# Kernel tuning notes

Hardware: AMD Instinct MI355X
Metric: run time of the kernel (lower is better)

Reference implementation:

```python
import jax, jax.numpy as jnp
import numpy as np

N_ATOM_TYPES = 100
N_BOND_TYPES = 10
N_NODES = 10000
N_EDGES = 320000
N_CAND = 100000
HID = 256
N_MP = 3


def setup_inputs() -> dict:
    key = jax.random.key(0)
    ks = jax.random.split(key, 16)
    d = HID
    inp = {
        "atom_types": jax.random.randint(ks[0], (N_NODES,), 0, N_ATOM_TYPES),
        "bond_types": jax.random.randint(ks[1], (N_EDGES,), 0, N_BOND_TYPES),
        "edge_index": jax.random.randint(ks[2], (2, N_EDGES), 0, N_NODES),
        "candidates": jax.random.randint(ks[3], (N_CAND, 2), 0, N_NODES),
        # parameters (weights stored as [in, out]; bias [out])
        "atom_embed": jax.random.normal(ks[4], (N_ATOM_TYPES, d)) * 0.02,
        "atom_W": jax.random.normal(ks[5], (d, d)) / np.sqrt(d),
        "atom_b": jnp.zeros((d,)),
        "bond_embed": jax.random.normal(ks[6], (N_BOND_TYPES, d)) * 0.02,
        "bond_W": jax.random.normal(ks[7], (d, d)) / np.sqrt(d),
        "bond_b": jnp.zeros((d,)),
        "conv_W": jax.random.normal(ks[8], (N_MP, d, d)) / np.sqrt(d),
        "conv_b": jnp.zeros((N_MP, d)),
        "s_W1": jax.random.normal(ks[9], (2 * d, d)) / np.sqrt(2 * d),
        "s_b1": jnp.zeros((d,)),
        "s_W2": jax.random.normal(ks[10], (d, 1)) / np.sqrt(d),
        "s_b2": jnp.zeros((1,)),
    }
    return inp


def _wln_forward(atom_types, bond_types, edge_index, candidates,
                 atom_embed, atom_W, atom_b, bond_embed, bond_W, bond_b,
                 conv_W, conv_b, s_W1, s_b1, s_W2, s_b2):
    # encoders
    h = atom_embed[atom_types] @ atom_W + atom_b            # [N, d]
    e = bond_embed[bond_types] @ bond_W + bond_b            # [E, d] (unused downstream, as in the original forward)
    del e

    src, dst = edge_index[0], edge_index[1]
    n = h.shape[0]
    ones = jnp.ones((src.shape[0],), dtype=h.dtype)
    deg_out = jax.ops.segment_sum(ones, src, num_segments=n)
    deg_in = jax.ops.segment_sum(ones, dst, num_segments=n)
    norm_src = jnp.where(deg_out > 0, deg_out ** -0.5, 0.0)[:, None]  # [N,1]
    norm_dst = jnp.where(deg_in > 0, deg_in ** -0.5, 0.0)[:, None]

    # message passing: DGL GraphConv norm='both' + ReLU
    for i in range(conv_W.shape[0]):
        m = (h * norm_src)[src]                             # [E, d]
        agg = jax.ops.segment_sum(m, dst, num_segments=n)   # [N, d]
        h = jax.nn.relu((agg * norm_dst) @ conv_W[i] + conv_b[i])

    # batched candidate scorer: gather + concat + 2-layer MLP
    u, v = candidates[:, 0], candidates[:, 1]
    pair = jnp.concatenate([h[u], h[v]], axis=-1)           # [C, 2d]
    hid = jax.nn.relu(pair @ s_W1 + s_b1)                   # [C, d]
    scores = hid @ s_W2 + s_b2                              # [C, 1]
    return scores.squeeze(-1)                               # [C]


def reference(atom_types, bond_types, edge_index, candidates,
              atom_embed, atom_W, atom_b, bond_embed, bond_W, bond_b,
              conv_W, conv_b, s_W1, s_b1, s_W2, s_b2):
    return _wln_forward(atom_types, bond_types, edge_index, candidates,
                        atom_embed, atom_W, atom_b, bond_embed, bond_W, bond_b,
                        conv_W, conv_b, s_W1, s_b1, s_W2, s_b2)
```

## Files before the change

kernel.cpp:

```cpp
#include <hip/hip_runtime.h>

#define N_NODES 10000
#define N_EDGES 320000
#define N_CAND  100000
#define HID     256
#define N_MP    3
#define N_ATYPE 100

static __device__ __forceinline__ float relu_f(float x) { return x > 0.f ? x : 0.f; }

static __device__ __forceinline__ void gemm_core(
    const float* __restrict__ A, const float* __restrict__ B,
    const float* __restrict__ bias, const float* __restrict__ scale,
    float* __restrict__ C, int M, int mb, int nb,
    int kbase, int klen, int doRelu)
{
    __shared__ float As[32][64];
    __shared__ float Bs[32][64];

    int tid = threadIdx.x;
    int tx = tid & 15;
    int ty = tid >> 4;

    float acc[4][4] = {};

    for (int k0 = kbase; k0 < kbase + klen; k0 += 32) {
        #pragma unroll
        for (int p = 0; p < 2; ++p) {
            int flat = p * 256 + tid;
            int row  = flat >> 3;
            int kc   = flat & 7;
            float4 av = make_float4(0.f, 0.f, 0.f, 0.f);
            if (mb + row < M)
                av = *(const float4*)(A + (size_t)(mb + row) * 256 + k0 + kc * 4);
            int sc = row ^ (kc << 2);
            As[kc * 4 + 0][sc] = av.x;
            As[kc * 4 + 1][sc] = av.y;
            As[kc * 4 + 2][sc] = av.z;
            As[kc * 4 + 3][sc] = av.w;
        }
        #pragma unroll
        for (int p = 0; p < 2; ++p) {
            int flat = p * 256 + tid;
            int row  = flat >> 4;
            int c    = flat & 15;
            *(float4*)(&Bs[row][c * 4]) =
                *(const float4*)(B + (size_t)(k0 + row) * 256 + nb + c * 4);
        }
        __syncthreads();

        #pragma unroll 16
        for (int k = 0; k < 32; ++k) {
            float4 a4 = *(const float4*)(&As[k][(ty * 4) ^ ((k >> 2) << 2)]);
            float4 b4 = *(const float4*)(&Bs[k][tx * 4]);
            float a[4] = {a4.x, a4.y, a4.z, a4.w};
            float b[4] = {b4.x, b4.y, b4.z, b4.w};
            #pragma unroll
            for (int i = 0; i < 4; ++i)
                #pragma unroll
                for (int j = 0; j < 4; ++j)
                    acc[i][j] = fmaf(a[i], b[j], acc[i][j]);
        }
        __syncthreads();
    }

    float bvv[4] = {0.f, 0.f, 0.f, 0.f};
    if (bias) {
        float4 bv = *(const float4*)(bias + nb + tx * 4);
        bvv[0] = bv.x; bvv[1] = bv.y; bvv[2] = bv.z; bvv[3] = bv.w;
    }
    #pragma unroll
    for (int i = 0; i < 4; ++i) {
        int row = mb + ty * 4 + i;
        if (row >= M) continue;
        float sc = scale ? scale[row] : 1.0f;
        float r[4];
        #pragma unroll
        for (int j = 0; j < 4; ++j) {
            r[j] = acc[i][j] + bvv[j];
            if (doRelu) r[j] = relu_f(r[j]);
            r[j] *= sc;
        }
        *(float4*)(C + (size_t)row * 256 + nb + tx * 4) =
            make_float4(r[0], r[1], r[2], r[3]);
    }
}

__global__ __launch_bounds__(256) void k_gemm(
    const float* __restrict__ A, const float* __restrict__ B,
    const float* __restrict__ bias, float* __restrict__ C,
    int M, int doRelu)
{
    gemm_core(A, B, bias, nullptr, C, M, blockIdx.x * 64, blockIdx.y * 64,
              0, 256, doRelu);
}

__global__ __launch_bounds__(256) void k_gemm_conv(
    const float* __restrict__ A, const float* __restrict__ B,
    float* __restrict__ C0, float* __restrict__ C1, int M)
{
    int bid = blockIdx.x;
    int l = bid & 7;
    int r = bid >> 3;
    int ks = r & 1;
    int y  = (r >> 1) & 3;
    int g  = r >> 3;
    int x  = g * 8 + l;
    if (x * 64 >= M) return;
    float* C = ks ? C1 : C0;
    gemm_core(A, B, nullptr, nullptr, C, M, x * 64, y * 64, ks * 128, 128, 0);
}

__global__ __launch_bounds__(256) void k_combine(
    float* __restrict__ C0, const float* __restrict__ C1,
    const float* __restrict__ bias, const float* __restrict__ scale)
{
    int i = blockIdx.x * 256 + threadIdx.x;
    if (i >= N_NODES * 64) return;
    int row  = i >> 6;
    int col4 = i & 63;
    float4 a = ((const float4*)C0)[i];
    float4 b = ((const float4*)C1)[i];
    float4 bv = ((const float4*)bias)[col4];
    float sc = scale ? scale[row] : 1.0f;
    float4 r;
    r.x = relu_f(a.x + b.x + bv.x) * sc;
    r.y = relu_f(a.y + b.y + bv.y) * sc;
    r.z = relu_f(a.z + b.z + bv.z) * sc;
    r.w = relu_f(a.w + b.w + bv.w) * sc;
    ((float4*)C0)[i] = r;
}

__global__ __launch_bounds__(256) void k_gemm_pq(
    const float* __restrict__ A, const float* __restrict__ W1,
    float* __restrict__ P, float* __restrict__ Q, int M)
{
    int bid = blockIdx.x;
    int l = bid & 7;
    int r = bid >> 3;
    int y = r & 7;
    int g = r >> 3;
    int x = g * 8 + l;
    if (x * 64 >= M) return;
    int half = y >> 2;
    const float* B = W1 + (size_t)half * 256 * 256;
    float* C = half ? Q : P;
    gemm_core(A, B, nullptr, nullptr, C, M, x * 64, (y & 3) * 64, 0, 256, 0);
}

__global__ void k_hist(const int* __restrict__ ei,
                       int* __restrict__ dout, int* __restrict__ din)
{
    int e = blockIdx.x * blockDim.x + threadIdx.x;
    if (e >= N_EDGES) return;
    atomicAdd(&dout[ei[e]], 1);
    atomicAdd(&din[ei[N_EDGES + e]], 1);
}

__global__ void k_norm(const int* __restrict__ dout, const int* __restrict__ din,
                       float* __restrict__ ns, float* __restrict__ nd)
{
    int i = blockIdx.x * blockDim.x + threadIdx.x;
    if (i >= N_NODES) return;
    int o = dout[i], in = din[i];
    ns[i] = (o  > 0) ? (1.0f / sqrtf((float)o))  : 0.f;
    nd[i] = (in > 0) ? (1.0f / sqrtf((float)in)) : 0.f;
}

__global__ __launch_bounds__(256) void k_h0(const int* __restrict__ types,
                                            const float* __restrict__ E0,
                                            const float* __restrict__ ns,
                                            float* __restrict__ h)
{
    int node = blockIdx.x * 4 + (threadIdx.x >> 6);
    int lane = threadIdx.x & 63;
    if (node >= N_NODES) return;
    int t = types[node];
    float s = ns[node];
    float4 v = ((const float4*)E0)[t * 64 + lane];
    v.x *= s; v.y *= s; v.z *= s; v.w *= s;
    ((float4*)h)[node * 64 + lane] = v;
}

__global__ __launch_bounds__(1024) void k_scan(const int* __restrict__ deg,
                                               int* __restrict__ off, int n)
{
    __shared__ int part[1024];
    int t = threadIdx.x;
    int chunk = (n + 1023) / 1024;
    int base = t * chunk;
    int s = 0;
    for (int i = 0; i < chunk; ++i) {
        int idx = base + i;
        if (idx < n) s += deg[idx];
    }
    part[t] = s;
    __syncthreads();
    for (int d = 1; d < 1024; d <<= 1) {
        int v = (t >= d) ? part[t - d] : 0;
        __syncthreads();
        part[t] += v;
        __syncthreads();
    }
    int run = (t == 0) ? 0 : part[t - 1];
    if (t == 0) off[0] = 0;
    for (int i = 0; i < chunk; ++i) {
        int idx = base + i;
        if (idx < n) { run += deg[idx]; off[idx + 1] = run; }
    }
}

__global__ void k_fill(const int* __restrict__ ei, const int* __restrict__ off,
                       int* __restrict__ cur, int* __restrict__ csr)
{
    int e = blockIdx.x * blockDim.x + threadIdx.x;
    if (e >= N_EDGES) return;
    int d = ei[N_EDGES + e];
    int p = off[d] + atomicAdd(&cur[d], 1);
    csr[p] = ei[e];
}

__global__ __launch_bounds__(256) void k_agg(
    const float* __restrict__ h, const float* __restrict__ nd,
    const int* __restrict__ off, const int* __restrict__ csr,
    float* __restrict__ out)
{
    int bid  = blockIdx.x;
    int slot = bid & 7;
    int c    = slot >> 1;
    int p    = ((bid >> 3) << 1) | (slot & 1);
    int wave = threadIdx.x >> 6;
    int lane = threadIdx.x & 63;
    int wi   = p * 4 + wave;
    int col  = c * 64 + lane;

    for (int node = wi; node < N_NODES; node += 2048) {
        int s0 = off[node], s1 = off[node + 1];
        float a0 = 0.f, a1 = 0.f, a2 = 0.f, a3 = 0.f;
        float a4 = 0.f, a5 = 0.f, a6 = 0.f, a7 = 0.f;
        int e = s0;
        for (; e + 8 <= s1; e += 8) {
            int i0 = csr[e],     i1 = csr[e + 1], i2 = csr[e + 2], i3 = csr[e + 3];
            int i4 = csr[e + 4], i5 = csr[e + 5], i6 = csr[e + 6], i7 = csr[e + 7];
            float v0 = h[(size_t)i0 * 256 + col];
            float v1 = h[(size_t)i1 * 256 + col];
            float v2 = h[(size_t)i2 * 256 + col];
            float v3 = h[(size_t)i3 * 256 + col];
            float v4 = h[(size_t)i4 * 256 + col];
            float v5 = h[(size_t)i5 * 256 + col];
            float v6 = h[(size_t)i6 * 256 + col];
            float v7 = h[(size_t)i7 * 256 + col];
            a0 += v0; a1 += v1; a2 += v2; a3 += v3;
            a4 += v4; a5 += v5; a6 += v6; a7 += v7;
        }
        for (; e < s1; ++e)
            a0 += h[(size_t)csr[e] * 256 + col];
        float s = ((a0 + a1) + (a2 + a3)) + ((a4 + a5) + (a6 + a7));
        out[(size_t)node * 256 + col] = s * nd[node];
    }
}

__global__ __launch_bounds__(256) void k_score_part(
    const int* __restrict__ cand, const float* __restrict__ P,
    const float* __restrict__ Q, const float* __restrict__ b1,
    const float* __restrict__ W2, float* __restrict__ part)
{
    int bid = blockIdx.x;
    int c   = bid & 7;
    int grp = bid >> 3;
    int cd  = grp * 256 + threadIdx.x;
    if (cd >= N_CAND) return;

    int u = cand[2 * cd];
    int v = cand[2 * cd + 1];
    const float4* P4 = (const float4*)P;
    const float4* Q4 = (const float4*)Q;
    const float4* B4 = (const float4*)b1;
    const float4* W4 = (const float4*)W2;
    size_t pb = (size_t)u * 64 + c * 8;
    size_t qb = (size_t)v * 64 + c * 8;

    float4 p[8], q[8];
    #pragma unroll
    for (int i = 0; i < 8; ++i) p[i] = P4[pb + i];
    #pragma unroll
    for (int i = 0; i < 8; ++i) q[i] = Q4[qb + i];

    float acc = 0.f;
    #pragma unroll
    for (int i = 0; i < 8; ++i) {
        float4 b = B4[c * 8 + i];
        float4 w = W4[c * 8 + i];
        acc = fmaf(relu_f(p[i].x + q[i].x + b.x), w.x, acc);
        acc = fmaf(relu_f(p[i].y + q[i].y + b.y), w.y, acc);
        acc = fmaf(relu_f(p[i].z + q[i].z + b.z), w.z, acc);
        acc = fmaf(relu_f(p[i].w + q[i].w + b.w), w.w, acc);
    }
    part[(size_t)c * N_CAND + cd] = acc;
}

__global__ void k_sred(const float* __restrict__ part,
                       const float* __restrict__ b2, float* __restrict__ out)
{
    int i = blockIdx.x * 256 + threadIdx.x;
    if (i >= N_CAND) return;
    float s = b2[0];
    #pragma unroll
    for (int c = 0; c < 8; ++c) s += part[(size_t)c * N_CAND + i];
    out[i] = s;
}

extern "C" void kernel_launch(void* const* d_in, const int* in_sizes, int n_in,
                              void* d_out, int out_size, void* d_ws, size_t ws_size,
                              hipStream_t stream)
{
    const int*   atom_types = (const int*)d_in[0];
    const int*   edge_index = (const int*)d_in[2];
    const int*   candidates = (const int*)d_in[3];
    const float* atom_embed = (const float*)d_in[4];
    const float* atom_W     = (const float*)d_in[5];
    const float* atom_b     = (const float*)d_in[6];
    const float* conv_W     = (const float*)d_in[10];
    const float* conv_b     = (const float*)d_in[11];
    const float* s_W1       = (const float*)d_in[12];
    const float* s_b1       = (const float*)d_in[13];
    const float* s_W2       = (const float*)d_in[14];
    const float* s_b2       = (const float*)d_in[15];
    float* out = (float*)d_out;

    char* w = (char*)d_ws;
    size_t o = 0;
    auto alloc = [&](size_t bytes) {
        void* p = w + o;
        o += (bytes + 255) & ~(size_t)255;
        return p;
    };
    float* h0   = (float*)alloc((size_t)N_NODES * HID * 4);
    float* h1   = (float*)alloc((size_t)N_NODES * HID * 4);
    float* agg  = (float*)alloc((size_t)N_NODES * HID * 4);
    float* ctmp = (float*)alloc((size_t)N_NODES * HID * 4);
    float* E0   = (float*)alloc((size_t)N_ATYPE * HID * 4);
    float* part = (float*)alloc((size_t)8 * N_CAND * 4);
    int*   ints = (int*)alloc((size_t)3 * N_NODES * 4);
    float* ns   = (float*)alloc((size_t)N_NODES * 4);
    float* nd   = (float*)alloc((size_t)N_NODES * 4);
    int*   off  = (int*)alloc((size_t)(N_NODES + 1) * 4);
    int*   csr  = (int*)alloc((size_t)N_EDGES * 4);
    int* dego = ints;
    int* degi = ints + N_NODES;
    int* cur  = ints + 2 * N_NODES;

    hipMemsetAsync(ints, 0, (size_t)3 * N_NODES * 4, stream);

    k_gemm<<<dim3(2, 4), 256, 0, stream>>>(atom_embed, atom_W, atom_b, E0, N_ATYPE, 0);

    k_hist<<<(N_EDGES + 255) / 256, 256, 0, stream>>>(edge_index, dego, degi);
    k_norm<<<(N_NODES + 255) / 256, 256, 0, stream>>>(dego, degi, ns, nd);
    k_h0<<<N_NODES / 4, 256, 0, stream>>>(atom_types, E0, ns, h0);
    k_scan<<<1, 1024, 0, stream>>>(degi, off, N_NODES);
    k_fill<<<(N_EDGES + 255) / 256, 256, 0, stream>>>(edge_index, off, cur, csr);

    const float* hc = h0;
    float* hn = h1;
    const int NF4 = N_NODES * 64;
    for (int i = 0; i < N_MP; ++i) {
        k_agg<<<2048, 256, 0, stream>>>(hc, nd, off, csr, agg);
        k_gemm_conv<<<1280, 256, 0, stream>>>(
            agg, conv_W + (size_t)i * HID * HID, hn, ctmp, N_NODES);
        const float* sc = (i < N_MP - 1) ? ns : nullptr;
        k_combine<<<(NF4 + 255) / 256, 256, 0, stream>>>(
            hn, ctmp, conv_b + (size_t)i * HID, sc);
        float* t = (float*)hc; hc = hn; hn = t;
    }
    float* P = agg;
    float* Q = hn;
    k_gemm_pq<<<1280, 256, 0, stream>>>(hc, s_W1, P, Q, N_NODES);

    k_score_part<<<3128, 256, 0, stream>>>(candidates, P, Q, s_b1, s_W2, part);
    k_sred<<<(N_CAND + 255) / 256, 256, 0, stream>>>(part, s_b2, out);
}
```

Baseline: 354.2 us.

## Replace FP32 SIMT GEMMs with split-bf16 MFMA GEMMs and fuse combine

The conv and scorer-projection GEMMs move from a scalar FP32 shared-memory kernel onto bf16 MFMA instructions. Each FP32 operand is split into high and low bf16 parts, and three MFMA products recover near-FP32 accuracy. The aggregation kernel now writes the split bf16 activations directly. The conv GEMM applies bias, ReLU and scale in its epilogue, which removes the split-K partial buffer and the separate combine kernel. This adds a weight-prep kernel and a split kernel before the PQ GEMM. The MFMA tiles read operands straight from global memory with no LDS staging, and the output stores are scalar and strided.

After: 356.8 us. About the same (+0.7%).

```diff
diff --git a/kernel.cpp b/kernel.cpp
--- a/kernel.cpp
+++ b/kernel.cpp
@@ -7,48 +7,53 @@
 #define N_MP    3
 #define N_ATYPE 100
 
+typedef short bf16x8 __attribute__((ext_vector_type(8)));
+typedef float f32x4  __attribute__((ext_vector_type(4)));
+
 static __device__ __forceinline__ float relu_f(float x) { return x > 0.f ? x : 0.f; }
 
-static __device__ __forceinline__ void gemm_core(
+static __device__ __forceinline__ void split_bf16(float s, unsigned short& hi,
+                                                  unsigned short& lo)
+{
+    unsigned u = __float_as_uint(s);
+    hi = (unsigned short)(u >> 16);
+    float rem = s - __uint_as_float(u & 0xffff0000u);
+    unsigned v = __float_as_uint(rem);
+    unsigned r = v + 0x7fffu + ((v >> 16) & 1u);
+    lo = (unsigned short)(r >> 16);
+}
+
+__global__ __launch_bounds__(256) void k_gemm(
     const float* __restrict__ A, const float* __restrict__ B,
-    const float* __restrict__ bias, const float* __restrict__ scale,
-    float* __restrict__ C, int M, int mb, int nb,
-    int kbase, int klen, int doRelu)
+    const float* __restrict__ bias, float* __restrict__ C,
+    int M, int doRelu)
 {
     __shared__ float As[32][64];
     __shared__ float Bs[32][64];
-
     int tid = threadIdx.x;
-    int tx = tid & 15;
-    int ty = tid >> 4;
-
+    int tx = tid & 15, ty = tid >> 4;
+    int mb = blockIdx.x * 64, nb = blockIdx.y * 64;
     float acc[4][4] = {};
-
-    for (int k0 = kbase; k0 < kbase + klen; k0 += 32) {
+    for (int k0 = 0; k0 < 256; k0 += 32) {
         #pragma unroll
         for (int p = 0; p < 2; ++p) {
             int flat = p * 256 + tid;
-            int row  = flat >> 3;
-            int kc   = flat & 7;
+            int row = flat >> 3, kc = flat & 7;
             float4 av = make_float4(0.f, 0.f, 0.f, 0.f);
             if (mb + row < M)
                 av = *(const float4*)(A + (size_t)(mb + row) * 256 + k0 + kc * 4);
             int sc = row ^ (kc << 2);
-            As[kc * 4 + 0][sc] = av.x;
-            As[kc * 4 + 1][sc] = av.y;
-            As[kc * 4 + 2][sc] = av.z;
-            As[kc * 4 + 3][sc] = av.w;
+            As[kc * 4 + 0][sc] = av.x; As[kc * 4 + 1][sc] = av.y;
+            As[kc * 4 + 2][sc] = av.z; As[kc * 4 + 3][sc] = av.w;
         }
         #pragma unroll
         for (int p = 0; p < 2; ++p) {
             int flat = p * 256 + tid;
-            int row  = flat >> 4;
-            int c    = flat & 15;
+            int row = flat >> 4, c = flat & 15;
             *(float4*)(&Bs[row][c * 4]) =
                 *(const float4*)(B + (size_t)(k0 + row) * 256 + nb + c * 4);
         }
         __syncthreads();
-
         #pragma unroll 16
         for (int k = 0; k < 32; ++k) {
             float4 a4 = *(const float4*)(&As[k][(ty * 4) ^ ((k >> 2) << 2)]);
@@ -63,89 +68,170 @@
         }
         __syncthreads();
     }
-
-    float bvv[4] = {0.f, 0.f, 0.f, 0.f};
-    if (bias) {
-        float4 bv = *(const float4*)(bias + nb + tx * 4);
-        bvv[0] = bv.x; bvv[1] = bv.y; bvv[2] = bv.z; bvv[3] = bv.w;
-    }
     #pragma unroll
     for (int i = 0; i < 4; ++i) {
         int row = mb + ty * 4 + i;
         if (row >= M) continue;
-        float sc = scale ? scale[row] : 1.0f;
         float r[4];
         #pragma unroll
         for (int j = 0; j < 4; ++j) {
-            r[j] = acc[i][j] + bvv[j];
+            r[j] = acc[i][j] + (bias ? bias[nb + tx * 4 + j] : 0.f);
             if (doRelu) r[j] = relu_f(r[j]);
-            r[j] *= sc;
         }
         *(float4*)(C + (size_t)row * 256 + nb + tx * 4) =
             make_float4(r[0], r[1], r[2], r[3]);
     }
 }
 
-__global__ __launch_bounds__(256) void k_gemm(
-    const float* __restrict__ A, const float* __restrict__ B,
-    const float* __restrict__ bias, float* __restrict__ C,
-    int M, int doRelu)
-{
-    gemm_core(A, B, bias, nullptr, C, M, blockIdx.x * 64, blockIdx.y * 64,
-              0, 256, doRelu);
-}
-
-__global__ __launch_bounds__(256) void k_gemm_conv(
-    const float* __restrict__ A, const float* __restrict__ B,
-    float* __restrict__ C0, float* __restrict__ C1, int M)
+__global__ __launch_bounds__(256) void k_prep_w(
+    const float* __restrict__ conv_W, const float* __restrict__ s_W1,
+    unsigned short* __restrict__ WTh, unsigned short* __restrict__ WTl)
 {
     int bid = blockIdx.x;
-    int l = bid & 7;
-    int r = bid >> 3;
-    int ks = r & 1;
-    int y  = (r >> 1) & 3;
-    int g  = r >> 3;
-    int x  = g * 8 + l;
-    if (x * 64 >= M) return;
-    float* C = ks ? C1 : C0;
-    gemm_core(A, B, nullptr, nullptr, C, M, x * 64, y * 64, ks * 128, 128, 0);
-}
-
-__global__ __launch_bounds__(256) void k_combine(
-    float* __restrict__ C0, const float* __restrict__ C1,
-    const float* __restrict__ bias, const float* __restrict__ scale)
+    int mat = bid >> 6;
+    int id  = (bid & 63) * 256 + threadIdx.x;
+    int k   = id >> 6;
+    int n4  = id & 63;
+    const float* src = (mat < 3) ? conv_W + (size_t)mat * 65536
+                                 : s_W1 + (size_t)(mat - 3) * 65536;
+    float4 w = *(const float4*)(src + (size_t)k * 256 + n4 * 4);
+    float ws[4] = {w.x, w.y, w.z, w.w};
+    #pragma unroll
+    for (int j = 0; j < 4; ++j) {
+        unsigned short hi, lo;
+        split_bf16(ws[j], hi, lo);
+        size_t idx = (size_t)mat * 65536 + (size_t)(n4 * 4 + j) * 256 + k;
+        WTh[idx] = hi;
+        WTl[idx] = lo;
+    }
+}
+
+__global__ __launch_bounds__(256) void k_split(
+    const float* __restrict__ h, unsigned short* __restrict__ Ah,
+    unsigned short* __restrict__ Al)
 {
     int i = blockIdx.x * 256 + threadIdx.x;
-    if (i >= N_NODES * 64) return;
-    int row  = i >> 6;
-    int col4 = i & 63;
-    float4 a = ((const float4*)C0)[i];
-    float4 b = ((const float4*)C1)[i];
-    float4 bv = ((const float4*)bias)[col4];
-    float sc = scale ? scale[row] : 1.0f;
-    float4 r;
-    r.x = relu_f(a.x + b.x + bv.x) * sc;
-    r.y = relu_f(a.y + b.y + bv.y) * sc;
-    r.z = relu_f(a.z + b.z + bv.z) * sc;
-    r.w = relu_f(a.w + b.w + bv.w) * sc;
-    ((float4*)C0)[i] = r;
-}
-
-__global__ __launch_bounds__(256) void k_gemm_pq(
-    const float* __restrict__ A, const float* __restrict__ W1,
-    float* __restrict__ P, float* __restrict__ Q, int M)
+    float4 v = ((const float4*)h)[i];
+    float vs[4] = {v.x, v.y, v.z, v.w};
+    unsigned short hs[4], ls[4];
+    #pragma unroll
+    for (int j = 0; j < 4; ++j) split_bf16(vs[j], hs[j], ls[j]);
+    ushort4 hv = make_ushort4(hs[0], hs[1], hs[2], hs[3]);
+    ushort4 lv = make_ushort4(ls[0], ls[1], ls[2], ls[3]);
+    ((ushort4*)Ah)[i] = hv;
+    ((ushort4*)Al)[i] = lv;
+}
+
+static __device__ __forceinline__ void mfma_tile(
+    const unsigned short* __restrict__ Ah, const unsigned short* __restrict__ Al,
+    const unsigned short* __restrict__ Wh, const unsigned short* __restrict__ Wl,
+    const float* __restrict__ bias, const float* __restrict__ scale,
+    float* __restrict__ C, int M, int mb, int nb, int doRelu)
+{
+    int l  = threadIdx.x & 63;
+    int li = l & 15;
+    int g  = l >> 4;
+
+    int r0 = mb + li;       if (r0 >= M) r0 = M - 1;
+    int r1 = mb + 16 + li;  if (r1 >= M) r1 = M - 1;
+    int c0 = nb + li;
+    int c1 = nb + 16 + li;
+
+    const unsigned short* pA0h = Ah + (size_t)r0 * 256 + g * 8;
+    const unsigned short* pA1h = Ah + (size_t)r1 * 256 + g * 8;
+    const unsigned short* pA0l = Al + (size_t)r0 * 256 + g * 8;
+    const unsigned short* pA1l = Al + (size_t)r1 * 256 + g * 8;
+    const unsigned short* pB0h = Wh + (size_t)c0 * 256 + g * 8;
+    const unsigned short* pB1h = Wh + (size_t)c1 * 256 + g * 8;
+    const unsigned short* pB0l = Wl + (size_t)c0 * 256 + g * 8;
+    const unsigned short* pB1l = Wl + (size_t)c1 * 256 + g * 8;
+
+    f32x4 acc00 = {0.f, 0.f, 0.f, 0.f};
+    f32x4 acc01 = {0.f, 0.f, 0.f, 0.f};
+    f32x4 acc10 = {0.f, 0.f, 0.f, 0.f};
+    f32x4 acc11 = {0.f, 0.f, 0.f, 0.f};
+
+    #pragma unroll
+    for (int ks = 0; ks < 8; ++ks) {
+        int o = ks * 32;
+        bf16x8 a0h = *(const bf16x8*)(pA0h + o);
+        bf16x8 a1h = *(const bf16x8*)(pA1h + o);
+        bf16x8 a0l = *(const bf16x8*)(pA0l + o);
+        bf16x8 a1l = *(const bf16x8*)(pA1l + o);
+        bf16x8 b0h = *(const bf16x8*)(pB0h + o);
+        bf16x8 b1h = *(const bf16x8*)(pB1h + o);
+        bf16x8 b0l = *(const bf16x8*)(pB0l + o);
+        bf16x8 b1l = *(const bf16x8*)(pB1l + o);
+
+        acc00 = __builtin_amdgcn_mfma_f32_16x16x32_bf16(a0h, b0h, acc00, 0, 0, 0);
+        acc01 = __builtin_amdgcn_mfma_f32_16x16x32_bf16(a0h, b1h, acc01, 0, 0, 0);
+        acc10 = __builtin_amdgcn_mfma_f32_16x16x32_bf16(a1h, b0h, acc10, 0, 0, 0);
+        acc11 = __builtin_amdgcn_mfma_f32_16x16x32_bf16(a1h, b1h, acc11, 0, 0, 0);
+
+        acc00 = __builtin_amdgcn_mfma_f32_16x16x32_bf16(a0h, b0l, acc00, 0, 0, 0);
+        acc01 = __builtin_amdgcn_mfma_f32_16x16x32_bf16(a0h, b1l, acc01, 0, 0, 0);
+        acc10 = __builtin_amdgcn_mfma_f32_16x16x32_bf16(a1h, b0l, acc10, 0, 0, 0);
+        acc11 = __builtin_amdgcn_mfma_f32_16x16x32_bf16(a1h, b1l, acc11, 0, 0, 0);
+
+        acc00 = __builtin_amdgcn_mfma_f32_16x16x32_bf16(a0l, b0h, acc00, 0, 0, 0);
+        acc01 = __builtin_amdgcn_mfma_f32_16x16x32_bf16(a0l, b1h, acc01, 0, 0, 0);
+        acc10 = __builtin_amdgcn_mfma_f32_16x16x32_bf16(a1l, b0h, acc10, 0, 0, 0);
+        acc11 = __builtin_amdgcn_mfma_f32_16x16x32_bf16(a1l, b1h, acc11, 0, 0, 0);
+    }
+
+    #pragma unroll
+    for (int rt = 0; rt < 2; ++rt) {
+        #pragma unroll
+        for (int ct = 0; ct < 2; ++ct) {
+            f32x4 a = rt ? (ct ? acc11 : acc10) : (ct ? acc01 : acc00);
+            int col = nb + ct * 16 + li;
+            float bv = bias ? bias[col] : 0.f;
+            #pragma unroll
+            for (int j = 0; j < 4; ++j) {
+                int row = mb + rt * 16 + g * 4 + j;
+                if (row >= M) continue;
+                float v = a[j] + bv;
+                if (doRelu) v = relu_f(v);
+                if (scale) v *= scale[row];
+                C[(size_t)row * 256 + col] = v;
+            }
+        }
+    }
+}
+
+__global__ __launch_bounds__(64) void k_gemm_conv_mfma(
+    const unsigned short* __restrict__ Ah, const unsigned short* __restrict__ Al,
+    const unsigned short* __restrict__ Wh, const unsigned short* __restrict__ Wl,
+    const float* __restrict__ bias, const float* __restrict__ scale,
+    float* __restrict__ C, int M)
 {
     int bid = blockIdx.x;
     int l = bid & 7;
     int r = bid >> 3;
     int y = r & 7;
-    int g = r >> 3;
-    int x = g * 8 + l;
-    if (x * 64 >= M) return;
-    int half = y >> 2;
-    const float* B = W1 + (size_t)half * 256 * 256;
-    float* C = half ? Q : P;
-    gemm_core(A, B, nullptr, nullptr, C, M, x * 64, (y & 3) * 64, 0, 256, 0);
+    int gx = r >> 3;
+    int x = gx * 8 + l;
+    if (x * 32 >= M) return;
+    mfma_tile(Ah, Al, Wh, Wl, bias, scale, C, M, x * 32, y * 32, 1);
+}
+
+__global__ __launch_bounds__(64) void k_gemm_pq_mfma(
+    const unsigned short* __restrict__ Ah, const unsigned short* __restrict__ Al,
+    const unsigned short* __restrict__ WTh, const unsigned short* __restrict__ WTl,
+    float* __restrict__ P, float* __restrict__ Q, int M)
+{
+    int bid = blockIdx.x;
+    int l = bid & 7;
+    int r = bid >> 3;
+    int y = r & 7;
+    int t = r >> 3;
+    int half = t & 1;
+    int gx = t >> 1;
+    int x = gx * 8 + l;
+    if (x * 32 >= M) return;
+    const unsigned short* wh = WTh + (size_t)(3 + half) * 65536;
+    const unsigned short* wl = WTl + (size_t)(3 + half) * 65536;
+    mfma_tile(Ah, Al, wh, wl, nullptr, nullptr, half ? Q : P, M, x * 32, y * 32, 0);
 }
 
 __global__ void k_hist(const int* __restrict__ ei,
@@ -223,7 +309,7 @@
 __global__ __launch_bounds__(256) void k_agg(
     const float* __restrict__ h, const float* __restrict__ nd,
     const int* __restrict__ off, const int* __restrict__ csr,
-    float* __restrict__ out)
+    unsigned short* __restrict__ Ah, unsigned short* __restrict__ Al)
 {
     int bid  = blockIdx.x;
     int slot = bid & 7;
@@ -255,8 +341,11 @@
         }
         for (; e < s1; ++e)
             a0 += h[(size_t)csr[e] * 256 + col];
-        float s = ((a0 + a1) + (a2 + a3)) + ((a4 + a5) + (a6 + a7));
-        out[(size_t)node * 256 + col] = s * nd[node];
+        float s = (((a0 + a1) + (a2 + a3)) + ((a4 + a5) + (a6 + a7))) * nd[node];
+        unsigned short hi, lo;
+        split_bf16(s, hi, lo);
+        Ah[(size_t)node * 256 + col] = hi;
+        Al[(size_t)node * 256 + col] = lo;
     }
 }
 
@@ -335,17 +424,21 @@
         o += (bytes + 255) & ~(size_t)255;
         return p;
     };
-    float* h0   = (float*)alloc((size_t)N_NODES * HID * 4);
-    float* h1   = (float*)alloc((size_t)N_NODES * HID * 4);
-    float* agg  = (float*)alloc((size_t)N_NODES * HID * 4);
-    float* ctmp = (float*)alloc((size_t)N_NODES * HID * 4);
-    float* E0   = (float*)alloc((size_t)N_ATYPE * HID * 4);
-    float* part = (float*)alloc((size_t)8 * N_CAND * 4);
-    int*   ints = (int*)alloc((size_t)3 * N_NODES * 4);
-    float* ns   = (float*)alloc((size_t)N_NODES * 4);
-    float* nd   = (float*)alloc((size_t)N_NODES * 4);
-    int*   off  = (int*)alloc((size_t)(N_NODES + 1) * 4);
-    int*   csr  = (int*)alloc((size_t)N_EDGES * 4);
+    float*          h0   = (float*)alloc((size_t)N_NODES * HID * 4);
+    float*          h1   = (float*)alloc((size_t)N_NODES * HID * 4);
+    float*          P    = (float*)alloc((size_t)N_NODES * HID * 4);
+    float*          Q    = (float*)alloc((size_t)N_NODES * HID * 4);
+    unsigned short* Ah   = (unsigned short*)alloc((size_t)N_NODES * HID * 2);
+    unsigned short* Al   = (unsigned short*)alloc((size_t)N_NODES * HID * 2);
+    unsigned short* WTh  = (unsigned short*)alloc((size_t)5 * 65536 * 2);
+    unsigned short* WTl  = (unsigned short*)alloc((size_t)5 * 65536 * 2);
+    float*          E0   = (float*)alloc((size_t)N_ATYPE * HID * 4);
+    float*          part = (float*)alloc((size_t)8 * N_CAND * 4);
+    int*            ints = (int*)alloc((size_t)3 * N_NODES * 4);
+    float*          ns   = (float*)alloc((size_t)N_NODES * 4);
+    float*          nd   = (float*)alloc((size_t)N_NODES * 4);
+    int*            off  = (int*)alloc((size_t)(N_NODES + 1) * 4);
+    int*            csr  = (int*)alloc((size_t)N_EDGES * 4);
     int* dego = ints;
     int* degi = ints + N_NODES;
     int* cur  = ints + 2 * N_NODES;
@@ -353,6 +446,7 @@
     hipMemsetAsync(ints, 0, (size_t)3 * N_NODES * 4, stream);
 
     k_gemm<<<dim3(2, 4), 256, 0, stream>>>(atom_embed, atom_W, atom_b, E0, N_ATYPE, 0);
+    k_prep_w<<<320, 256, 0, stream>>>(conv_W, s_W1, WTh, WTl);
 
     k_hist<<<(N_EDGES + 255) / 256, 256, 0, stream>>>(edge_index, dego, degi);
     k_norm<<<(N_NODES + 255) / 256, 256, 0, stream>>>(dego, degi, ns, nd);
@@ -362,19 +456,16 @@
 
     const float* hc = h0;
     float* hn = h1;
-    const int NF4 = N_NODES * 64;
     for (int i = 0; i < N_MP; ++i) {
-        k_agg<<<2048, 256, 0, stream>>>(hc, nd, off, csr, agg);
-        k_gemm_conv<<<1280, 256, 0, stream>>>(
-            agg, conv_W + (size_t)i * HID * HID, hn, ctmp, N_NODES);
+        k_agg<<<2048, 256, 0, stream>>>(hc, nd, off, csr, Ah, Al);
         const float* sc = (i < N_MP - 1) ? ns : nullptr;
-        k_combine<<<(NF4 + 255) / 256, 256, 0, stream>>>(
-            hn, ctmp, conv_b + (size_t)i * HID, sc);
+        k_gemm_conv_mfma<<<2560, 64, 0, stream>>>(
+            Ah, Al, WTh + (size_t)i * 65536, WTl + (size_t)i * 65536,
+            conv_b + (size_t)i * HID, sc, hn, N_NODES);
         float* t = (float*)hc; hc = hn; hn = t;
     }
-    float* P = agg;
-    float* Q = hn;
-    k_gemm_pq<<<1280, 256, 0, stream>>>(hc, s_W1, P, Q, N_NODES);
+    k_split<<<2500, 256, 0, stream>>>(hc, Ah, Al);
+    k_gemm_pq_mfma<<<5120, 64, 0, stream>>>(Ah, Al, WTh, WTl, P, Q, N_NODES);
 
     k_score_part<<<3128, 256, 0, stream>>>(candidates, P, Q, s_b1, s_W2, part);
     k_sred<<<(N_CAND + 255) / 256, 256, 0, stream>>>(part, s_b2, out);
```
